# Kernel tuning notes

Measured on AMD Instinct MI355X. Metric: run time of the kernel, lower is better.

The kernel has to match this reference:

```python
import jax, jax.numpy as jnp
import numpy as np

SEQ_LEN = 96      # args.seq_len (in_feats)
H_FEATS = 100
OUT_FEATS = 128
HEADS = 4
K = 64            # args.input_size = nodes per graph
B = 256           # number of graphs (batch_size)
N = K * B
DEG = 8
E = N * DEG
OUT_SIZE = 24     # args.output_size
NEG_SLOPE = 0.2   # PyG GATConv default


def setup_inputs() -> dict:
    key = jax.random.key(0)
    ks = jax.random.split(key, 20)
    s = 0.05
    x = jax.random.normal(ks[0], (N, SEQ_LEN), jnp.float32)
    # intra-graph random edges (dst repeated, src within same graph)
    dst = jnp.repeat(jnp.arange(N, dtype=jnp.int32), DEG)
    src = (dst // K) * K + jax.random.randint(ks[1], (E,), 0, K, dtype=jnp.int32)
    edge_index = jnp.stack([src, dst])
    batch = jnp.repeat(jnp.arange(B, dtype=jnp.int32), K)
    y = jax.random.normal(ks[2], (N, OUT_SIZE), jnp.float32)
    # GATConv 1: in=96 -> heads=4, ch=100
    W1 = jax.random.normal(ks[3], (SEQ_LEN, HEADS * H_FEATS), jnp.float32) * s
    as1 = jax.random.normal(ks[4], (HEADS, H_FEATS), jnp.float32) * s
    ad1 = jax.random.normal(ks[5], (HEADS, H_FEATS), jnp.float32) * s
    b1 = jnp.zeros((H_FEATS,), jnp.float32)
    # GATConv 2: in=100 -> heads=4, ch=128
    W2 = jax.random.normal(ks[6], (H_FEATS, HEADS * OUT_FEATS), jnp.float32) * s
    as2 = jax.random.normal(ks[7], (HEADS, OUT_FEATS), jnp.float32) * s
    ad2 = jax.random.normal(ks[8], (HEADS, OUT_FEATS), jnp.float32) * s
    b2 = jnp.zeros((OUT_FEATS,), jnp.float32)
    # per-node-index MLPs (batched over K)
    fw1 = jax.random.normal(ks[9], (K, OUT_FEATS, 64), jnp.float32) * s
    fb1 = jnp.zeros((K, 64), jnp.float32)
    fw2 = jax.random.normal(ks[10], (K, 64, OUT_SIZE), jnp.float32) * s
    fb2 = jnp.zeros((K, OUT_SIZE), jnp.float32)
    return dict(x=x, edge_index=edge_index, batch=batch, y=y,
                W1=W1, as1=as1, ad1=ad1, b1=b1,
                W2=W2, as2=as2, ad2=ad2, b2=b2,
                fw1=fw1, fb1=fb1, fw2=fw2, fb2=fb2)


def gat_conv(x, src, dst, W, a_src, a_dst, bias):
    # PyG GATConv (concat=False): linear -> per-edge attention -> softmax over
    # incoming edges of each dst -> weighted sum -> mean over heads + bias.
    n = x.shape[0]
    xl = (x @ W).reshape(n, HEADS, -1)                      # [N,H,C]
    al_src = jnp.sum(xl * a_src, axis=-1)                   # [N,H]
    al_dst = jnp.sum(xl * a_dst, axis=-1)                   # [N,H]
    alpha = jax.nn.leaky_relu(al_src[src] + al_dst[dst], NEG_SLOPE)  # [E,H]
    m = jax.ops.segment_max(alpha, dst, num_segments=n)
    ea = jnp.exp(alpha - m[dst])
    denom = jax.ops.segment_sum(ea, dst, num_segments=n)
    w = ea / (denom[dst] + 1e-16)                           # [E,H]
    msg = xl[src] * w[:, :, None]                           # [E,H,C]
    out = jax.ops.segment_sum(msg, dst, num_segments=n)     # [N,H,C]
    return out.mean(axis=1) + bias                          # concat=False


def reference(x, edge_index, batch, y, W1, as1, ad1, b1, W2, as2, ad2, b2, fw1, fb1, fw2, fb2):
    n = x.shape[0]
    src, dst = edge_index[0], edge_index[1]
    loop = jnp.arange(n, dtype=src.dtype)                   # GATConv adds self-loops
    src = jnp.concatenate([src, loop])
    dst = jnp.concatenate([dst, loop])
    h = jax.nn.elu(gat_conv(x, src, dst, W1, as1, ad1, b1))
    h = gat_conv(h, src, dst, W2, as2, ad2, b2)             # [N,128]
    # batch is sorted with K nodes per graph -> stacking == static reshape
    xg = h.reshape(B, K, OUT_FEATS).transpose(1, 0, 2)      # [K,B,128]
    hid = jax.nn.relu(jnp.einsum('kbi,kih->kbh', xg, fw1) + fb1[:, None, :])
    pred = jnp.einsum('kbh,kho->kbo', hid, fw2) + fb2[:, None, :]  # [K,B,out]
    yg = y.reshape(B, K, OUT_SIZE)                          # [B,K,out]
    return pred, yg
```

## Files before the change

kernel.cpp:

```cpp
#include <hip/hip_runtime.h>
#include <hip/hip_bf16.h>
#include <math.h>


#define N_NODES 16384
#define B_GRAPHS 256
#define K_NODES 64
#define DEG 8
#define NHEADS 4
#define C1 100
#define C2 128
#define IN_F 96
#define HID 64
#define OUT_SZ 24
#define PRED_ELEMS (K_NODES * B_GRAPHS * OUT_SZ)

#define W1T_ROWS 448
#define W1T_K    96
#define W2T_ROWS 528
#define W2T_K    128

using bf16 = __hip_bfloat16;
typedef __attribute__((ext_vector_type(8))) short          frag_ab;
typedef __attribute__((ext_vector_type(4))) float          frag_cd;
typedef unsigned short us8 __attribute__((ext_vector_type(8)));
typedef unsigned short us4 __attribute__((ext_vector_type(4)));

__device__ __forceinline__ float us2f(unsigned short u) {
  return __bfloat162float(__ushort_as_bfloat16(u));
}
__device__ __forceinline__ short f2bf_s(float f) {
  return __builtin_bit_cast(short, __float2bfloat16(f));
}

#define P1N  (W1T_ROWS * W1T_K)
#define P2N  (W2T_ROWS * W2T_K)
#define YG4  (PRED_ELEMS / 4)
#define FW1N (K_NODES * HID * C2)
#define FW2N (K_NODES * 32 * HID)
#define PREP_TOT (P1N + P2N + YG4 + FW1N + FW2N)

__global__ __launch_bounds__(256)
void prep(const float* __restrict__ W1, const float* __restrict__ W2,
          const float* __restrict__ y,
          const float* __restrict__ as1, const float* __restrict__ ad1,
          const float* __restrict__ as2, const float* __restrict__ ad2,
          const float* __restrict__ fw1, const float* __restrict__ fw2,
          bf16* __restrict__ W1t, bf16* __restrict__ W2t,
          bf16* __restrict__ fw1t, bf16* __restrict__ fw2t,
          float* __restrict__ yg) {
  int idx = blockIdx.x * 256 + threadIdx.x;
  if (idx < P1N) {
    int c = idx / W1T_K, k = idx - c * W1T_K;
    float v = 0.f;
    if (c < 400) {
      v = W1[(size_t)k * 400 + c];
    } else if (c < 408) {
      int h = (c - 400) & 3;
      const float* av = (c < 404) ? as1 : ad1;
      float s = 0.f;
#pragma unroll 4
      for (int q = 0; q < 100; ++q)
        s += W1[(size_t)k * 400 + h * 100 + q] * av[h * 100 + q];
      v = s;
    }
    W1t[idx] = __float2bfloat16(v);
  } else if (idx < P1N + P2N) {
    int i2 = idx - P1N;
    int c = i2 >> 7, kk = i2 & 127;
    float v = 0.f;
    if (c < 512) {
      if (kk < 100) v = W2[(size_t)kk * 512 + c];
    } else if (c < 520 && kk < 100) {
      int h = (c - 512) & 3;
      const float* av = (c < 516) ? as2 : ad2;
      float s = 0.f;
#pragma unroll 4
      for (int q = 0; q < 128; ++q)
        s += W2[(size_t)kk * 512 + h * 128 + q] * av[h * 128 + q];
      v = s;
    }
    W2t[i2] = __float2bfloat16(v);
  } else if (idx < P1N + P2N + YG4) {
    int j = idx - P1N - P2N;
    int i = j * 4;
    float4 v = *(const float4*)(y + i);
    v.x = __bfloat162float(__float2bfloat16(v.x));
    v.y = __bfloat162float(__float2bfloat16(v.y));
    v.z = __bfloat162float(__float2bfloat16(v.z));
    v.w = __bfloat162float(__float2bfloat16(v.w));
    *(float4*)(yg + i) = v;
  } else if (idx < P1N + P2N + YG4 + FW1N) {
    int i4 = idx - (P1N + P2N + YG4);
    int k = i4 >> 13, r = i4 & 8191, n = r >> 7, kk = r & 127;
    fw1t[i4] = __float2bfloat16(fw1[(size_t)k * (C2 * HID) + kk * HID + n]);
  } else {
    int i5 = idx - (P1N + P2N + YG4 + FW1N);
    if (i5 < FW2N) {
      int k = i5 >> 11, r = i5 & 2047, n = r >> 6, kk = r & 63;
      fw2t[i5] = __float2bfloat16(
          (n < OUT_SZ) ? fw2[(size_t)k * (HID * OUT_SZ) + kk * OUT_SZ + n] : 0.f);
    }
  }
}

__global__ __launch_bounds__(512)
void gat_fused(const float* __restrict__ x,
               const bf16* __restrict__ W1t, const bf16* __restrict__ W2t,
               const int* __restrict__ esrc,
               const float* __restrict__ b1, const float* __restrict__ b2,
               bf16* __restrict__ h2t) {
  constexpr int LDA1 = IN_F + 8;
  constexpr int LDA2 = 136;
  constexpr int LDT  = 72;

  __shared__ __align__(16) short          As[64 * LDA2];
  __shared__ __align__(16) unsigned short xs[W2T_ROWS * LDT];
  __shared__ __align__(16) short          Ps[NHEADS * 64 * LDT];
  __shared__ float bia1[C1], bia2[C2];
  __shared__ int   edg[K_NODES * DEG];

  const int g = blockIdx.x;
  const int t = threadIdx.x;
  const int wv = t >> 6;
  const int l  = t & 63;
  const int lm = l & 15;
  const int lk = (l >> 4) * 8;
  const int rq = (l >> 4) * 4;

  {
    constexpr int QR = IN_F / 4;
    for (int idx = t; idx < 64 * QR; idx += 512) {
      int m = idx / QR, q = idx - m * QR;
      const float4 v = *(const float4*)(x + ((size_t)(g * 64 + m) * IN_F + q * 4));
      short* d = &As[m * LDA1 + q * 4];
      d[0] = f2bf_s(v.x); d[1] = f2bf_s(v.y); d[2] = f2bf_s(v.z); d[3] = f2bf_s(v.w);
    }
  }
  if (t < C1) bia1[t] = b1[t];
  else if (t >= 128 && t < 128 + C2) bia2[t - 128] = b2[t - 128];
  if (t < K_NODES * DEG) edg[t] = esrc[g * K_NODES * DEG + t] & (K_NODES - 1);
  for (int idx = t; idx < NHEADS * 64 * LDT / 8; idx += 512)
    *(us8*)&Ps[idx * 8] = (us8)0;
  __syncthreads();

  if (wv < 7) {
    const int n0 = wv * 64;
    frag_cd acc[4][4] = {};
#pragma unroll
    for (int ks = 0; ks < IN_F; ks += 32) {
      frag_ab b[4];
#pragma unroll
      for (int nt = 0; nt < 4; ++nt)
        b[nt] = *(const frag_ab*)((const short*)W1t +
                                  (size_t)(n0 + nt * 16 + lm) * W1T_K + ks + lk);
#pragma unroll
      for (int mt = 0; mt < 4; ++mt) {
        frag_ab a = *(const frag_ab*)&As[(mt * 16 + lm) * LDA1 + ks + lk];
#pragma unroll
        for (int nt = 0; nt < 4; ++nt)
          acc[mt][nt] = __builtin_amdgcn_mfma_f32_16x16x32_bf16(a, b[nt],
                                                                acc[mt][nt], 0, 0, 0);
      }
    }
#pragma unroll
    for (int mt = 0; mt < 4; ++mt)
#pragma unroll
      for (int nt = 0; nt < 4; ++nt) {
        const int c4 = n0 + nt * 16 + lm;
        us4 o;
#pragma unroll
        for (int r = 0; r < 4; ++r) o[r] = (unsigned short)f2bf_s(acc[mt][nt][r]);
        *(us4*)&xs[c4 * LDT + mt * 16 + rq] = o;
      }
  }
  __syncthreads();

  if (t < 256) {
    const int n = t >> 2, h = t & 3;
    const float ad = us2f(xs[(404 + h) * LDT + n]);
    int   sv[9];
    float a[9];
#pragma unroll
    for (int j = 0; j < 8; ++j) sv[j] = edg[n * DEG + j];
    sv[8] = n;
#pragma unroll
    for (int j = 0; j < 9; ++j) {
      float v = us2f(xs[(400 + h) * LDT + sv[j]]) + ad;
      a[j] = (v >= 0.f) ? v : 0.2f * v;
    }
    float m = -1e30f;
#pragma unroll
    for (int j = 0; j < 9; ++j) m = fmaxf(m, a[j]);
    float s = 0.f;
#pragma unroll
    for (int j = 0; j < 9; ++j) { a[j] = __expf(a[j] - m); s += a[j]; }
    const float inv = 1.f / (s + 1e-16f);
    short* prow = &Ps[(h * 64 + n) * LDT];
#pragma unroll
    for (int j = 0; j < 9; ++j) {
      float tw = a[j];
#pragma unroll
      for (int i = 0; i < 9; ++i)
        if (i != j && sv[i] == sv[j]) tw += a[i];
      prow[sv[j]] = f2bf_s(tw * inv);
    }
  } else {
    for (int i = t - 256; i < 64 * 28; i += 256) {
      int m = i / 28, kk = 100 + (i - m * 28);
      As[m * LDA2 + kk] = 0;
    }
  }
  __syncthreads();

  {
    const int mw = (wv & 3) * 16;
    const int cg = wv >> 2;
    const int ntb = cg * 4;
    const int nte = (cg == 0) ? 4 : 7;
    frag_cd acc[4] = {};
#pragma unroll
    for (int h = 0; h < NHEADS; ++h)
#pragma unroll
      for (int ks = 0; ks < 64; ks += 32) {
        frag_ab a = *(const frag_ab*)&Ps[(h * 64 + mw + lm) * LDT + ks + lk];
        for (int nt = ntb; nt < nte; ++nt) {
          frag_ab b = *(const frag_ab*)&xs[(h * C1 + nt * 16 + lm) * LDT + ks + lk];
          acc[nt - ntb] = __builtin_amdgcn_mfma_f32_16x16x32_bf16(a, b,
                                                                  acc[nt - ntb], 0, 0, 0);
      }
    }
    for (int nt = ntb; nt < nte; ++nt) {
      const int c = nt * 16 + lm;
      if (c < C1) {
        const float bc = bia1[c];
#pragma unroll
        for (int r = 0; r < 4; ++r) {
          float vv = acc[nt - ntb][r] * 0.25f + bc;
          vv = (vv > 0.f) ? vv : (__expf(vv) - 1.f);
          As[(mw + rq + r) * LDA2 + c] = f2bf_s(vv);
        }
      }
    }
  }
  __syncthreads();

  {
    const int n0 = wv * 64;
    frag_cd acc[4][4] = {};
    frag_cd accL[4] = {};
#pragma unroll
    for (int ks = 0; ks < 128; ks += 32) {
      frag_ab b[4];
#pragma unroll
      for (int nt = 0; nt < 4; ++nt)
        b[nt] = *(const frag_ab*)((const short*)W2t +
                                  (size_t)(n0 + nt * 16 + lm) * W2T_K + ks + lk);
      frag_ab bl;
      if (wv == 0)
        bl = *(const frag_ab*)((const short*)W2t +
                               (size_t)(512 + lm) * W2T_K + ks + lk);
#pragma unroll
      for (int mt = 0; mt < 4; ++mt) {
        frag_ab a = *(const frag_ab*)&As[(mt * 16 + lm) * LDA2 + ks + lk];
#pragma unroll
        for (int nt = 0; nt < 4; ++nt)
          acc[mt][nt] = __builtin_amdgcn_mfma_f32_16x16x32_bf16(a, b[nt],
                                                                acc[mt][nt], 0, 0, 0);
        if (wv == 0)
          accL[mt] = __builtin_amdgcn_mfma_f32_16x16x32_bf16(a, bl, accL[mt], 0, 0, 0);
      }
    }
#pragma unroll
    for (int mt = 0; mt < 4; ++mt)
#pragma unroll
      for (int nt = 0; nt < 4; ++nt) {
        const int c4 = n0 + nt * 16 + lm;
        us4 o;
#pragma unroll
        for (int r = 0; r < 4; ++r) o[r] = (unsigned short)f2bf_s(acc[mt][nt][r]);
        *(us4*)&xs[c4 * LDT + mt * 16 + rq] = o;
      }
    if (wv == 0) {
#pragma unroll
      for (int mt = 0; mt < 4; ++mt) {
        us4 o;
#pragma unroll
        for (int r = 0; r < 4; ++r) o[r] = (unsigned short)f2bf_s(accL[mt][r]);
        *(us4*)&xs[(512 + lm) * LDT + mt * 16 + rq] = o;
      }
    }
  }
  __syncthreads();

  if (t < 256) {
    const int n = t >> 2, h = t & 3;
    const float ad = us2f(xs[(516 + h) * LDT + n]);
    int   sv[9];
    float a[9];
#pragma unroll
    for (int j = 0; j < 8; ++j) sv[j] = edg[n * DEG + j];
    sv[8] = n;
#pragma unroll
    for (int j = 0; j < 9; ++j) {
      float v = us2f(xs[(512 + h) * LDT + sv[j]]) + ad;
      a[j] = (v >= 0.f) ? v : 0.2f * v;
    }
    float m = -1e30f;
#pragma unroll
    for (int j = 0; j < 9; ++j) m = fmaxf(m, a[j]);
    float s = 0.f;
#pragma unroll
    for (int j = 0; j < 9; ++j) { a[j] = __expf(a[j] - m); s += a[j]; }
    const float inv = 1.f / (s + 1e-16f);
    short* prow = &Ps[(h * 64 + n) * LDT];
#pragma unroll
    for (int j = 0; j < 9; ++j) {
      float tw = a[j];
#pragma unroll
      for (int i = 0; i < 9; ++i)
        if (i != j && sv[i] == sv[j]) tw += a[i];
      prow[sv[j]] = f2bf_s(tw * inv);
    }
  }
  __syncthreads();

  {
    const int mw = (wv & 3) * 16;
    const int cg = wv >> 2;
    const int ntb = cg * 4;
    frag_cd acc[4] = {};
#pragma unroll
    for (int h = 0; h < NHEADS; ++h)
#pragma unroll
      for (int ks = 0; ks < 64; ks += 32) {
        frag_ab a = *(const frag_ab*)&Ps[(h * 64 + mw + lm) * LDT + ks + lk];
#pragma unroll
        for (int nt = 0; nt < 4; ++nt) {
          frag_ab b = *(const frag_ab*)&xs[(h * C2 + (ntb + nt) * 16 + lm) * LDT + ks + lk];
          acc[nt] = __builtin_amdgcn_mfma_f32_16x16x32_bf16(a, b, acc[nt], 0, 0, 0);
        }
      }
    unsigned short* outp = (unsigned short*)h2t;
#pragma unroll
    for (int nt = 0; nt < 4; ++nt) {
      const int c = (ntb + nt) * 16 + lm;
      const float bc = bia2[c];
#pragma unroll
      for (int r = 0; r < 4; ++r) {
        float vv = acc[nt][r] * 0.25f + bc;
        outp[((size_t)(mw + rq + r) * B_GRAPHS + g) * C2 + c] =
            (unsigned short)f2bf_s(vv);
      }
    }
  }
}

__global__ __launch_bounds__(256)
void mlp_mfma(const bf16* __restrict__ h2t,
              const bf16* __restrict__ fw1t, const float* __restrict__ fb1,
              const bf16* __restrict__ fw2t, const float* __restrict__ fb2,
              float* __restrict__ pred) {
  constexpr int LDH = HID + 8;
  __shared__ __align__(16) short Hs[64 * LDH];

  const int k  = blockIdx.x & 63;
  const int ms = blockIdx.x >> 6;
  const int t  = threadIdx.x;
  const int wv = t >> 6;
  const int l  = t & 63;
  const int lm = l & 15;
  const int lk = (l >> 4) * 8;
  const int rq = (l >> 4) * 4;

  const unsigned short* A  = (const unsigned short*)h2t +
                             ((size_t)k * B_GRAPHS + ms * 64) * C2;
  const unsigned short* B1 = (const unsigned short*)fw1t + (size_t)k * (HID * C2);

  frag_cd acc[4] = {};
#pragma unroll
  for (int ks = 0; ks < C2; ks += 32) {
    frag_ab a = *(const frag_ab*)(A + (size_t)(wv * 16 + lm) * C2 + ks + lk);
#pragma unroll
    for (int nt = 0; nt < 4; ++nt) {
      frag_ab b = *(const frag_ab*)(B1 + (size_t)(nt * 16 + lm) * C2 + ks + lk);
      acc[nt] = __builtin_amdgcn_mfma_f32_16x16x32_bf16(a, b, acc[nt], 0, 0, 0);
    }
  }
#pragma unroll
  for (int nt = 0; nt < 4; ++nt) {
    const int j  = nt * 16 + lm;
    const float bj = fb1[k * HID + j];
#pragma unroll
    for (int r = 0; r < 4; ++r) {
      const int m = wv * 16 + rq + r;
      Hs[m * LDH + j] = f2bf_s(fmaxf(acc[nt][r] + bj, 0.f));
    }
  }
  __syncthreads();

  const unsigned short* B2 = (const unsigned short*)fw2t + (size_t)k * (32 * HID);
  frag_cd acc2[2] = {};
#pragma unroll
  for (int ks = 0; ks < HID; ks += 32) {
    frag_ab a = *(const frag_ab*)&Hs[(wv * 16 + lm) * LDH + ks + lk];
#pragma unroll
    for (int nt = 0; nt < 2; ++nt) {
      frag_ab b = *(const frag_ab*)(B2 + (size_t)(nt * 16 + lm) * HID + ks + lk);
      acc2[nt] = __builtin_amdgcn_mfma_f32_16x16x32_bf16(a, b, acc2[nt], 0, 0, 0);
    }
  }
#pragma unroll
  for (int nt = 0; nt < 2; ++nt) {
    const int q = nt * 16 + lm;
    if (q < OUT_SZ) {
      const float bq = fb2[k * OUT_SZ + q];
#pragma unroll
      for (int r = 0; r < 4; ++r) {
        const int m = wv * 16 + rq + r;
        pred[((size_t)k * B_GRAPHS + ms * 64 + m) * OUT_SZ + q] = acc2[nt][r] + bq;
      }
    }
  }
}

extern "C" void kernel_launch(void* const* d_in, const int* in_sizes, int n_in,
                              void* d_out, int out_size, void* d_ws, size_t ws_size,
                              hipStream_t stream) {
  const float* x   = (const float*)d_in[0];
  const int*   ei  = (const int*)d_in[1];
  const float* y   = (const float*)d_in[3];
  const float* W1  = (const float*)d_in[4];
  const float* as1 = (const float*)d_in[5];
  const float* ad1 = (const float*)d_in[6];
  const float* b1  = (const float*)d_in[7];
  const float* W2  = (const float*)d_in[8];
  const float* as2 = (const float*)d_in[9];
  const float* ad2 = (const float*)d_in[10];
  const float* b2  = (const float*)d_in[11];
  const float* fw1 = (const float*)d_in[12];
  const float* fb1 = (const float*)d_in[13];
  const float* fw2 = (const float*)d_in[14];
  const float* fb2 = (const float*)d_in[15];

  bf16* h2t  = (bf16*)d_ws;
  bf16* W1t  = h2t + (size_t)N_NODES * C2;
  bf16* W2t  = W1t + P1N;
  bf16* fw1t = W2t + P2N;
  bf16* fw2t = fw1t + FW1N;

  float* out = (float*)d_out;

  prep<<<(PREP_TOT + 255) / 256, 256, 0, stream>>>(
      W1, W2, y, as1, ad1, as2, ad2, fw1, fw2, W1t, W2t, fw1t, fw2t,
      out + PRED_ELEMS);

  gat_fused<<<B_GRAPHS, 512, 0, stream>>>(x, W1t, W2t, ei, b1, b2, h2t);

  mlp_mfma<<<K_NODES * 4, 256, 0, stream>>>(h2t, fw1t, fb1, fw2t, fb2, out);
}
```

Baseline: 118.5 us.

## Fuse prep, GAT and MLP kernels into one cooperative kernel with grid syncs

Merges the three launches (weight prep, fused GAT, per-node MLP) into a single cooperative kernel of 256 blocks. Prep work is done in a grid-stride loop while each block stages its graph inputs, and grid-wide syncs replace the kernel boundaries before the GAT GEMMs and before the MLP. The MLP stage is remapped onto 8 waves per block and reuses the As shared buffer. This removes launch overhead and inter-kernel gaps, but adds grid-barrier cost and requires all 256 blocks to be co-resident.

```diff
diff --git a/kernel.cpp b/kernel.cpp
--- a/kernel.cpp
+++ b/kernel.cpp
@@ -1,6 +1,9 @@
 #include <hip/hip_runtime.h>
 #include <hip/hip_bf16.h>
+#include <hip/hip_cooperative_groups.h>
 #include <math.h>
+
+namespace cg = cooperative_groups;
 
 
 #define N_NODES 16384
@@ -40,79 +43,23 @@
 #define FW2N (K_NODES * 32 * HID)
 #define PREP_TOT (P1N + P2N + YG4 + FW1N + FW2N)
 
-__global__ __launch_bounds__(256)
-void prep(const float* __restrict__ W1, const float* __restrict__ W2,
-          const float* __restrict__ y,
-          const float* __restrict__ as1, const float* __restrict__ ad1,
-          const float* __restrict__ as2, const float* __restrict__ ad2,
-          const float* __restrict__ fw1, const float* __restrict__ fw2,
-          bf16* __restrict__ W1t, bf16* __restrict__ W2t,
-          bf16* __restrict__ fw1t, bf16* __restrict__ fw2t,
-          float* __restrict__ yg) {
-  int idx = blockIdx.x * 256 + threadIdx.x;
-  if (idx < P1N) {
-    int c = idx / W1T_K, k = idx - c * W1T_K;
-    float v = 0.f;
-    if (c < 400) {
-      v = W1[(size_t)k * 400 + c];
-    } else if (c < 408) {
-      int h = (c - 400) & 3;
-      const float* av = (c < 404) ? as1 : ad1;
-      float s = 0.f;
-#pragma unroll 4
-      for (int q = 0; q < 100; ++q)
-        s += W1[(size_t)k * 400 + h * 100 + q] * av[h * 100 + q];
-      v = s;
-    }
-    W1t[idx] = __float2bfloat16(v);
-  } else if (idx < P1N + P2N) {
-    int i2 = idx - P1N;
-    int c = i2 >> 7, kk = i2 & 127;
-    float v = 0.f;
-    if (c < 512) {
-      if (kk < 100) v = W2[(size_t)kk * 512 + c];
-    } else if (c < 520 && kk < 100) {
-      int h = (c - 512) & 3;
-      const float* av = (c < 516) ? as2 : ad2;
-      float s = 0.f;
-#pragma unroll 4
-      for (int q = 0; q < 128; ++q)
-        s += W2[(size_t)kk * 512 + h * 128 + q] * av[h * 128 + q];
-      v = s;
-    }
-    W2t[i2] = __float2bfloat16(v);
-  } else if (idx < P1N + P2N + YG4) {
-    int j = idx - P1N - P2N;
-    int i = j * 4;
-    float4 v = *(const float4*)(y + i);
-    v.x = __bfloat162float(__float2bfloat16(v.x));
-    v.y = __bfloat162float(__float2bfloat16(v.y));
-    v.z = __bfloat162float(__float2bfloat16(v.z));
-    v.w = __bfloat162float(__float2bfloat16(v.w));
-    *(float4*)(yg + i) = v;
-  } else if (idx < P1N + P2N + YG4 + FW1N) {
-    int i4 = idx - (P1N + P2N + YG4);
-    int k = i4 >> 13, r = i4 & 8191, n = r >> 7, kk = r & 127;
-    fw1t[i4] = __float2bfloat16(fw1[(size_t)k * (C2 * HID) + kk * HID + n]);
-  } else {
-    int i5 = idx - (P1N + P2N + YG4 + FW1N);
-    if (i5 < FW2N) {
-      int k = i5 >> 11, r = i5 & 2047, n = r >> 6, kk = r & 63;
-      fw2t[i5] = __float2bfloat16(
-          (n < OUT_SZ) ? fw2[(size_t)k * (HID * OUT_SZ) + kk * OUT_SZ + n] : 0.f);
-    }
-  }
-}
-
 __global__ __launch_bounds__(512)
-void gat_fused(const float* __restrict__ x,
-               const bf16* __restrict__ W1t, const bf16* __restrict__ W2t,
-               const int* __restrict__ esrc,
-               const float* __restrict__ b1, const float* __restrict__ b2,
-               bf16* __restrict__ h2t) {
+void fused_all(const float* __restrict__ x, const int* __restrict__ esrc,
+               const float* __restrict__ y,
+               const float* __restrict__ W1, const float* __restrict__ as1,
+               const float* __restrict__ ad1, const float* __restrict__ b1,
+               const float* __restrict__ W2, const float* __restrict__ as2,
+               const float* __restrict__ ad2, const float* __restrict__ b2,
+               const float* __restrict__ fw1, const float* __restrict__ fb1,
+               const float* __restrict__ fw2, const float* __restrict__ fb2,
+               bf16* __restrict__ W1t, bf16* __restrict__ W2t,
+               bf16* __restrict__ fw1t, bf16* __restrict__ fw2t,
+               bf16* __restrict__ h2t,
+               float* __restrict__ yg, float* __restrict__ pred) {
   constexpr int LDA1 = IN_F + 8;
   constexpr int LDA2 = 136;
   constexpr int LDT  = 72;
+  constexpr int LDH  = 72;
 
   __shared__ __align__(16) short          As[64 * LDA2];
   __shared__ __align__(16) unsigned short xs[W2T_ROWS * LDT];
@@ -142,7 +89,61 @@
   if (t < K_NODES * DEG) edg[t] = esrc[g * K_NODES * DEG + t] & (K_NODES - 1);
   for (int idx = t; idx < NHEADS * 64 * LDT / 8; idx += 512)
     *(us8*)&Ps[idx * 8] = (us8)0;
-  __syncthreads();
+
+  for (int idx = g * 512 + t; idx < PREP_TOT; idx += B_GRAPHS * 512) {
+    if (idx < P1N) {
+      int c = idx / W1T_K, k = idx - c * W1T_K;
+      float v = 0.f;
+      if (c < 400) {
+        v = W1[(size_t)k * 400 + c];
+      } else if (c < 408) {
+        int h = (c - 400) & 3;
+        const float* av = (c < 404) ? as1 : ad1;
+        float s = 0.f;
+#pragma unroll 4
+        for (int q = 0; q < 100; ++q)
+          s += W1[(size_t)k * 400 + h * 100 + q] * av[h * 100 + q];
+        v = s;
+      }
+      W1t[idx] = __float2bfloat16(v);
+    } else if (idx < P1N + P2N) {
+      int i2 = idx - P1N;
+      int c = i2 >> 7, kk = i2 & 127;
+      float v = 0.f;
+      if (c < 512) {
+        if (kk < 100) v = W2[(size_t)kk * 512 + c];
+      } else if (c < 520 && kk < 100) {
+        int h = (c - 512) & 3;
+        const float* av = (c < 516) ? as2 : ad2;
+        float s = 0.f;
+#pragma unroll 4
+        for (int q = 0; q < 128; ++q)
+          s += W2[(size_t)kk * 512 + h * 128 + q] * av[h * 128 + q];
+        v = s;
+      }
+      W2t[i2] = __float2bfloat16(v);
+    } else if (idx < P1N + P2N + YG4) {
+      int j = idx - P1N - P2N;
+      int i = j * 4;
+      float4 v = *(const float4*)(y + i);
+      v.x = __bfloat162float(__float2bfloat16(v.x));
+      v.y = __bfloat162float(__float2bfloat16(v.y));
+      v.z = __bfloat162float(__float2bfloat16(v.z));
+      v.w = __bfloat162float(__float2bfloat16(v.w));
+      *(float4*)(yg + i) = v;
+    } else if (idx < P1N + P2N + YG4 + FW1N) {
+      int i4 = idx - (P1N + P2N + YG4);
+      int k = i4 >> 13, r = i4 & 8191, n = r >> 7, kk = r & 127;
+      fw1t[i4] = __float2bfloat16(fw1[(size_t)k * (C2 * HID) + kk * HID + n]);
+    } else {
+      int i5 = idx - (P1N + P2N + YG4 + FW1N);
+      int k = i5 >> 11, r = i5 & 2047, n = r >> 6, kk = r & 63;
+      fw2t[i5] = __float2bfloat16(
+          (n < OUT_SZ) ? fw2[(size_t)k * (HID * OUT_SZ) + kk * OUT_SZ + n] : 0.f);
+    }
+  }
+  __threadfence();
+  cg::this_grid().sync();
 
   if (wv < 7) {
     const int n0 = wv * 64;
@@ -215,9 +216,9 @@
 
   {
     const int mw = (wv & 3) * 16;
-    const int cg = wv >> 2;
-    const int ntb = cg * 4;
-    const int nte = (cg == 0) ? 4 : 7;
+    const int cg2 = wv >> 2;
+    const int ntb = cg2 * 4;
+    const int nte = (cg2 == 0) ? 4 : 7;
     frag_cd acc[4] = {};
 #pragma unroll
     for (int h = 0; h < NHEADS; ++h)
@@ -327,8 +328,8 @@
 
   {
     const int mw = (wv & 3) * 16;
-    const int cg = wv >> 2;
-    const int ntb = cg * 4;
+    const int cg2 = wv >> 2;
+    const int ntb = cg2 * 4;
     frag_cd acc[4] = {};
 #pragma unroll
     for (int h = 0; h < NHEADS; ++h)
@@ -354,71 +355,56 @@
       }
     }
   }
-}
-
-__global__ __launch_bounds__(256)
-void mlp_mfma(const bf16* __restrict__ h2t,
-              const bf16* __restrict__ fw1t, const float* __restrict__ fb1,
-              const bf16* __restrict__ fw2t, const float* __restrict__ fb2,
-              float* __restrict__ pred) {
-  constexpr int LDH = HID + 8;
-  __shared__ __align__(16) short Hs[64 * LDH];
-
-  const int k  = blockIdx.x & 63;
-  const int ms = blockIdx.x >> 6;
-  const int t  = threadIdx.x;
-  const int wv = t >> 6;
-  const int l  = t & 63;
-  const int lm = l & 15;
-  const int lk = (l >> 4) * 8;
-  const int rq = (l >> 4) * 4;
-
-  const unsigned short* A  = (const unsigned short*)h2t +
-                             ((size_t)k * B_GRAPHS + ms * 64) * C2;
-  const unsigned short* B1 = (const unsigned short*)fw1t + (size_t)k * (HID * C2);
-
-  frag_cd acc[4] = {};
-#pragma unroll
-  for (int ks = 0; ks < C2; ks += 32) {
-    frag_ab a = *(const frag_ab*)(A + (size_t)(wv * 16 + lm) * C2 + ks + lk);
-#pragma unroll
-    for (int nt = 0; nt < 4; ++nt) {
-      frag_ab b = *(const frag_ab*)(B1 + (size_t)(nt * 16 + lm) * C2 + ks + lk);
-      acc[nt] = __builtin_amdgcn_mfma_f32_16x16x32_bf16(a, b, acc[nt], 0, 0, 0);
-    }
-  }
-#pragma unroll
-  for (int nt = 0; nt < 4; ++nt) {
-    const int j  = nt * 16 + lm;
-    const float bj = fb1[k * HID + j];
-#pragma unroll
-    for (int r = 0; r < 4; ++r) {
-      const int m = wv * 16 + rq + r;
-      Hs[m * LDH + j] = f2bf_s(fmaxf(acc[nt][r] + bj, 0.f));
-    }
-  }
-  __syncthreads();
-
-  const unsigned short* B2 = (const unsigned short*)fw2t + (size_t)k * (32 * HID);
-  frag_cd acc2[2] = {};
-#pragma unroll
-  for (int ks = 0; ks < HID; ks += 32) {
-    frag_ab a = *(const frag_ab*)&Hs[(wv * 16 + lm) * LDH + ks + lk];
+  __threadfence();
+  cg::this_grid().sync();
+
+  {
+    const int k  = blockIdx.x & 63;
+    const int ms = blockIdx.x >> 6;
+    const int mt = wv >> 1;
+    const int hf = wv & 1;
+
+    const unsigned short* A  = (const unsigned short*)h2t +
+                               ((size_t)k * B_GRAPHS + ms * 64) * C2;
+    const unsigned short* B1 = (const unsigned short*)fw1t + (size_t)k * (HID * C2);
+
+    frag_cd acc[2] = {};
+#pragma unroll
+    for (int ks = 0; ks < C2; ks += 32) {
+      frag_ab a = *(const frag_ab*)(A + (size_t)(mt * 16 + lm) * C2 + ks + lk);
+#pragma unroll
+      for (int nt = 0; nt < 2; ++nt) {
+        frag_ab b = *(const frag_ab*)(B1 + (size_t)((hf * 2 + nt) * 16 + lm) * C2 + ks + lk);
+        acc[nt] = __builtin_amdgcn_mfma_f32_16x16x32_bf16(a, b, acc[nt], 0, 0, 0);
+      }
+    }
 #pragma unroll
     for (int nt = 0; nt < 2; ++nt) {
-      frag_ab b = *(const frag_ab*)(B2 + (size_t)(nt * 16 + lm) * HID + ks + lk);
-      acc2[nt] = __builtin_amdgcn_mfma_f32_16x16x32_bf16(a, b, acc2[nt], 0, 0, 0);
-    }
-  }
-#pragma unroll
-  for (int nt = 0; nt < 2; ++nt) {
-    const int q = nt * 16 + lm;
+      const int j  = (hf * 2 + nt) * 16 + lm;
+      const float bj = fb1[k * HID + j];
+#pragma unroll
+      for (int r = 0; r < 4; ++r) {
+        const int m = mt * 16 + rq + r;
+        As[m * LDH + j] = f2bf_s(fmaxf(acc[nt][r] + bj, 0.f));
+      }
+    }
+    __syncthreads();
+
+    const unsigned short* B2 = (const unsigned short*)fw2t + (size_t)k * (32 * HID);
+    frag_cd acc2 = {};
+#pragma unroll
+    for (int ks = 0; ks < HID; ks += 32) {
+      frag_ab a = *(const frag_ab*)&As[(mt * 16 + lm) * LDH + ks + lk];
+      frag_ab b = *(const frag_ab*)(B2 + (size_t)(hf * 16 + lm) * HID + ks + lk);
+      acc2 = __builtin_amdgcn_mfma_f32_16x16x32_bf16(a, b, acc2, 0, 0, 0);
+    }
+    const int q = hf * 16 + lm;
     if (q < OUT_SZ) {
       const float bq = fb2[k * OUT_SZ + q];
 #pragma unroll
       for (int r = 0; r < 4; ++r) {
-        const int m = wv * 16 + rq + r;
-        pred[((size_t)k * B_GRAPHS + ms * 64 + m) * OUT_SZ + q] = acc2[nt][r] + bq;
+        const int m = mt * 16 + rq + r;
+        pred[((size_t)k * B_GRAPHS + ms * 64 + m) * OUT_SZ + q] = acc2[r] + bq;
       }
     }
   }
@@ -449,13 +435,18 @@
   bf16* fw1t = W2t + P2N;
   bf16* fw2t = fw1t + FW1N;
 
-  float* out = (float*)d_out;
-
-  prep<<<(PREP_TOT + 255) / 256, 256, 0, stream>>>(
-      W1, W2, y, as1, ad1, as2, ad2, fw1, fw2, W1t, W2t, fw1t, fw2t,
-      out + PRED_ELEMS);
-
-  gat_fused<<<B_GRAPHS, 512, 0, stream>>>(x, W1t, W2t, ei, b1, b2, h2t);
-
-  mlp_mfma<<<K_NODES * 4, 256, 0, stream>>>(h2t, fw1t, fb1, fw2t, fb2, out);
+  float* out  = (float*)d_out;
+  float* pred = out;
+  float* yg   = out + PRED_ELEMS;
+
+  void* args[] = {
+    (void*)&x, (void*)&ei, (void*)&y,
+    (void*)&W1, (void*)&as1, (void*)&ad1, (void*)&b1,
+    (void*)&W2, (void*)&as2, (void*)&ad2, (void*)&b2,
+    (void*)&fw1, (void*)&fb1, (void*)&fw2, (void*)&fb2,
+    (void*)&W1t, (void*)&W2t, (void*)&fw1t, (void*)&fw2t, (void*)&h2t,
+    (void*)&yg, (void*)&pred
+  };
+  hipLaunchCooperativeKernel((void*)fused_all, dim3(B_GRAPHS), dim3(512),
+                             args, 0, stream);
 }
```

Result: slower. 286.2 us (+141.5%).

## Remove prep kernel; convert weights inside GAT and MLP kernels

Applied to the files above, without the earlier changes.

Drops the separate weight-preparation kernel. The GAT kernel now reads fp32 W1/W2 directly with strided scalar loads and computes the attention-projection rows into shared memory per block. The MLP kernel stages transposed bf16 copies of fw1/fw2 in shared memory and also handles the y-to-bf16 round trip. This removes one launch and the intermediate round-trip through global memory, but every block redoes the weight conversion, and W1/W2 are now gathered with uncoalesced strided loads inside the MFMA loop.

```diff
diff --git a/kernel.cpp b/kernel.cpp
--- a/kernel.cpp
+++ b/kernel.cpp
@@ -14,11 +14,7 @@
 #define HID 64
 #define OUT_SZ 24
 #define PRED_ELEMS (K_NODES * B_GRAPHS * OUT_SZ)
-
-#define W1T_ROWS 448
-#define W1T_K    96
-#define W2T_ROWS 528
-#define W2T_K    128
+#define YG4 (PRED_ELEMS / 4)
 
 using bf16 = __hip_bfloat16;
 typedef __attribute__((ext_vector_type(8))) short          frag_ab;
@@ -33,90 +29,24 @@
   return __builtin_bit_cast(short, __float2bfloat16(f));
 }
 
-#define P1N  (W1T_ROWS * W1T_K)
-#define P2N  (W2T_ROWS * W2T_K)
-#define YG4  (PRED_ELEMS / 4)
-#define FW1N (K_NODES * HID * C2)
-#define FW2N (K_NODES * 32 * HID)
-#define PREP_TOT (P1N + P2N + YG4 + FW1N + FW2N)
-
-__global__ __launch_bounds__(256)
-void prep(const float* __restrict__ W1, const float* __restrict__ W2,
-          const float* __restrict__ y,
-          const float* __restrict__ as1, const float* __restrict__ ad1,
-          const float* __restrict__ as2, const float* __restrict__ ad2,
-          const float* __restrict__ fw1, const float* __restrict__ fw2,
-          bf16* __restrict__ W1t, bf16* __restrict__ W2t,
-          bf16* __restrict__ fw1t, bf16* __restrict__ fw2t,
-          float* __restrict__ yg) {
-  int idx = blockIdx.x * 256 + threadIdx.x;
-  if (idx < P1N) {
-    int c = idx / W1T_K, k = idx - c * W1T_K;
-    float v = 0.f;
-    if (c < 400) {
-      v = W1[(size_t)k * 400 + c];
-    } else if (c < 408) {
-      int h = (c - 400) & 3;
-      const float* av = (c < 404) ? as1 : ad1;
-      float s = 0.f;
-#pragma unroll 4
-      for (int q = 0; q < 100; ++q)
-        s += W1[(size_t)k * 400 + h * 100 + q] * av[h * 100 + q];
-      v = s;
-    }
-    W1t[idx] = __float2bfloat16(v);
-  } else if (idx < P1N + P2N) {
-    int i2 = idx - P1N;
-    int c = i2 >> 7, kk = i2 & 127;
-    float v = 0.f;
-    if (c < 512) {
-      if (kk < 100) v = W2[(size_t)kk * 512 + c];
-    } else if (c < 520 && kk < 100) {
-      int h = (c - 512) & 3;
-      const float* av = (c < 516) ? as2 : ad2;
-      float s = 0.f;
-#pragma unroll 4
-      for (int q = 0; q < 128; ++q)
-        s += W2[(size_t)kk * 512 + h * 128 + q] * av[h * 128 + q];
-      v = s;
-    }
-    W2t[i2] = __float2bfloat16(v);
-  } else if (idx < P1N + P2N + YG4) {
-    int j = idx - P1N - P2N;
-    int i = j * 4;
-    float4 v = *(const float4*)(y + i);
-    v.x = __bfloat162float(__float2bfloat16(v.x));
-    v.y = __bfloat162float(__float2bfloat16(v.y));
-    v.z = __bfloat162float(__float2bfloat16(v.z));
-    v.w = __bfloat162float(__float2bfloat16(v.w));
-    *(float4*)(yg + i) = v;
-  } else if (idx < P1N + P2N + YG4 + FW1N) {
-    int i4 = idx - (P1N + P2N + YG4);
-    int k = i4 >> 13, r = i4 & 8191, n = r >> 7, kk = r & 127;
-    fw1t[i4] = __float2bfloat16(fw1[(size_t)k * (C2 * HID) + kk * HID + n]);
-  } else {
-    int i5 = idx - (P1N + P2N + YG4 + FW1N);
-    if (i5 < FW2N) {
-      int k = i5 >> 11, r = i5 & 2047, n = r >> 6, kk = r & 63;
-      fw2t[i5] = __float2bfloat16(
-          (n < OUT_SZ) ? fw2[(size_t)k * (HID * OUT_SZ) + kk * OUT_SZ + n] : 0.f);
-    }
-  }
-}
-
 __global__ __launch_bounds__(512)
 void gat_fused(const float* __restrict__ x,
-               const bf16* __restrict__ W1t, const bf16* __restrict__ W2t,
+               const float* __restrict__ W1, const float* __restrict__ W2,
                const int* __restrict__ esrc,
-               const float* __restrict__ b1, const float* __restrict__ b2,
+               const float* __restrict__ as1, const float* __restrict__ ad1,
+               const float* __restrict__ b1,
+               const float* __restrict__ as2, const float* __restrict__ ad2,
+               const float* __restrict__ b2,
                bf16* __restrict__ h2t) {
   constexpr int LDA1 = IN_F + 8;
   constexpr int LDA2 = 136;
   constexpr int LDT  = 72;
 
   __shared__ __align__(16) short          As[64 * LDA2];
-  __shared__ __align__(16) unsigned short xs[W2T_ROWS * LDT];
+  __shared__ __align__(16) unsigned short xs[528 * LDT];
   __shared__ __align__(16) short          Ps[NHEADS * 64 * LDT];
+  __shared__ __align__(16) short          Wsd1[8 * 96];
+  __shared__ __align__(16) short          Wsd2[8 * 128];
   __shared__ float bia1[C1], bia2[C2];
   __shared__ int   edg[K_NODES * DEG];
 
@@ -142,6 +72,28 @@
   if (t < K_NODES * DEG) edg[t] = esrc[g * K_NODES * DEG + t] & (K_NODES - 1);
   for (int idx = t; idx < NHEADS * 64 * LDT / 8; idx += 512)
     *(us8*)&Ps[idx * 8] = (us8)0;
+  for (int e = t; e < 8 * 96; e += 512) {
+    int cc = e / 96, k = e - cc * 96;
+    int h = cc & 3;
+    const float* av = (cc < 4) ? as1 : ad1;
+    float s = 0.f;
+#pragma unroll 4
+    for (int c = 0; c < 100; ++c)
+      s += W1[(size_t)k * 400 + h * 100 + c] * av[h * 100 + c];
+    Wsd1[cc * 96 + k] = f2bf_s(s);
+  }
+  for (int e = t; e < 8 * 128; e += 512) {
+    int cc = e >> 7, kk = e & 127;
+    float s = 0.f;
+    if (kk < 100) {
+      int h = cc & 3;
+      const float* av = (cc < 4) ? as2 : ad2;
+#pragma unroll 4
+      for (int c = 0; c < 128; ++c)
+        s += W2[(size_t)kk * 512 + h * 128 + c] * av[h * 128 + c];
+    }
+    Wsd2[cc * 128 + kk] = f2bf_s(s);
+  }
   __syncthreads();
 
   if (wv < 7) {
@@ -151,9 +103,20 @@
     for (int ks = 0; ks < IN_F; ks += 32) {
       frag_ab b[4];
 #pragma unroll
-      for (int nt = 0; nt < 4; ++nt)
-        b[nt] = *(const frag_ab*)((const short*)W1t +
-                                  (size_t)(n0 + nt * 16 + lm) * W1T_K + ks + lk);
+      for (int nt = 0; nt < 4; ++nt) {
+        const int c = n0 + nt * 16 + lm;
+        frag_ab bb;
+        if (c < 400) {
+#pragma unroll
+          for (int j = 0; j < 8; ++j)
+            bb[j] = f2bf_s(W1[(size_t)(ks + lk + j) * 400 + c]);
+        } else if (c < 408) {
+          bb = *(const frag_ab*)&Wsd1[(c - 400) * 96 + ks + lk];
+        } else {
+          bb = (frag_ab)(short)0;
+        }
+        b[nt] = bb;
+      }
 #pragma unroll
       for (int mt = 0; mt < 4; ++mt) {
         frag_ab a = *(const frag_ab*)&As[(mt * 16 + lm) * LDA1 + ks + lk];
@@ -215,9 +178,9 @@
 
   {
     const int mw = (wv & 3) * 16;
-    const int cg = wv >> 2;
-    const int ntb = cg * 4;
-    const int nte = (cg == 0) ? 4 : 7;
+    const int cg2 = wv >> 2;
+    const int ntb = cg2 * 4;
+    const int nte = (cg2 == 0) ? 4 : 7;
     frag_cd acc[4] = {};
 #pragma unroll
     for (int h = 0; h < NHEADS; ++h)
@@ -253,13 +216,19 @@
     for (int ks = 0; ks < 128; ks += 32) {
       frag_ab b[4];
 #pragma unroll
-      for (int nt = 0; nt < 4; ++nt)
-        b[nt] = *(const frag_ab*)((const short*)W2t +
-                                  (size_t)(n0 + nt * 16 + lm) * W2T_K + ks + lk);
-      frag_ab bl;
-      if (wv == 0)
-        bl = *(const frag_ab*)((const short*)W2t +
-                               (size_t)(512 + lm) * W2T_K + ks + lk);
+      for (int nt = 0; nt < 4; ++nt) {
+        const int c = n0 + nt * 16 + lm;
+        frag_ab bb;
+#pragma unroll
+        for (int j = 0; j < 8; ++j) {
+          const int kk = ks + lk + j;
+          bb[j] = (kk < 100) ? f2bf_s(W2[(size_t)kk * 512 + c]) : (short)0;
+        }
+        b[nt] = bb;
+      }
+      frag_ab bl = (frag_ab)(short)0;
+      if (wv == 0 && lm < 8)
+        bl = *(const frag_ab*)&Wsd2[lm * 128 + ks + lk];
 #pragma unroll
       for (int mt = 0; mt < 4; ++mt) {
         frag_ab a = *(const frag_ab*)&As[(mt * 16 + lm) * LDA2 + ks + lk];
@@ -327,8 +296,8 @@
 
   {
     const int mw = (wv & 3) * 16;
-    const int cg = wv >> 2;
-    const int ntb = cg * 4;
+    const int cg2 = wv >> 2;
+    const int ntb = cg2 * 4;
     frag_cd acc[4] = {};
 #pragma unroll
     for (int h = 0; h < NHEADS; ++h)
@@ -358,10 +327,15 @@
 
 __global__ __launch_bounds__(256)
 void mlp_mfma(const bf16* __restrict__ h2t,
-              const bf16* __restrict__ fw1t, const float* __restrict__ fb1,
-              const bf16* __restrict__ fw2t, const float* __restrict__ fb2,
-              float* __restrict__ pred) {
-  constexpr int LDH = HID + 8;
+              const float* __restrict__ fw1, const float* __restrict__ fb1,
+              const float* __restrict__ fw2, const float* __restrict__ fb2,
+              const float* __restrict__ y,
+              float* __restrict__ yg, float* __restrict__ pred) {
+  constexpr int LDB1 = C2 + 8;
+  constexpr int LDB2 = HID + 8;
+  constexpr int LDH  = HID + 8;
+  __shared__ __align__(16) short B1[HID * LDB1];
+  __shared__ __align__(16) short B2[32 * LDB2];
   __shared__ __align__(16) short Hs[64 * LDH];
 
   const int k  = blockIdx.x & 63;
@@ -373,18 +347,41 @@
   const int lk = (l >> 4) * 8;
   const int rq = (l >> 4) * 4;
 
-  const unsigned short* A  = (const unsigned short*)h2t +
-                             ((size_t)k * B_GRAPHS + ms * 64) * C2;
-  const unsigned short* B1 = (const unsigned short*)fw1t + (size_t)k * (HID * C2);
+  const unsigned short* A = (const unsigned short*)h2t +
+                            ((size_t)k * B_GRAPHS + ms * 64) * C2;
+
+  frag_ab a_pre[4];
+#pragma unroll
+  for (int ksi = 0; ksi < 4; ++ksi)
+    a_pre[ksi] = *(const frag_ab*)(A + (size_t)(wv * 16 + lm) * C2 + ksi * 32 + lk);
+
+  for (int idx = t; idx < C2 * HID; idx += 256) {
+    int kk = idx >> 6, n = idx & 63;
+    B1[n * LDB1 + kk] = f2bf_s(fw1[(size_t)k * (C2 * HID) + idx]);
+  }
+  for (int idx = t; idx < HID * 32; idx += 256) {
+    int kk = idx >> 5, n = idx & 31;
+    B2[n * LDB2 + kk] = f2bf_s(
+        (n < OUT_SZ) ? fw2[(size_t)k * (HID * OUT_SZ) + kk * OUT_SZ + n] : 0.f);
+  }
+  for (int j = blockIdx.x * 256 + t; j < YG4; j += 256 * 256) {
+    int i = j * 4;
+    float4 v = *(const float4*)(y + i);
+    v.x = __bfloat162float(__float2bfloat16(v.x));
+    v.y = __bfloat162float(__float2bfloat16(v.y));
+    v.z = __bfloat162float(__float2bfloat16(v.z));
+    v.w = __bfloat162float(__float2bfloat16(v.w));
+    *(float4*)(yg + i) = v;
+  }
+  __syncthreads();
 
   frag_cd acc[4] = {};
 #pragma unroll
-  for (int ks = 0; ks < C2; ks += 32) {
-    frag_ab a = *(const frag_ab*)(A + (size_t)(wv * 16 + lm) * C2 + ks + lk);
+  for (int ksi = 0; ksi < 4; ++ksi) {
 #pragma unroll
     for (int nt = 0; nt < 4; ++nt) {
-      frag_ab b = *(const frag_ab*)(B1 + (size_t)(nt * 16 + lm) * C2 + ks + lk);
-      acc[nt] = __builtin_amdgcn_mfma_f32_16x16x32_bf16(a, b, acc[nt], 0, 0, 0);
+      frag_ab b = *(const frag_ab*)&B1[(nt * 16 + lm) * LDB1 + ksi * 32 + lk];
+      acc[nt] = __builtin_amdgcn_mfma_f32_16x16x32_bf16(a_pre[ksi], b, acc[nt], 0, 0, 0);
     }
   }
 #pragma unroll
@@ -399,14 +396,13 @@
   }
   __syncthreads();
 
-  const unsigned short* B2 = (const unsigned short*)fw2t + (size_t)k * (32 * HID);
   frag_cd acc2[2] = {};
 #pragma unroll
   for (int ks = 0; ks < HID; ks += 32) {
     frag_ab a = *(const frag_ab*)&Hs[(wv * 16 + lm) * LDH + ks + lk];
 #pragma unroll
     for (int nt = 0; nt < 2; ++nt) {
-      frag_ab b = *(const frag_ab*)(B2 + (size_t)(nt * 16 + lm) * HID + ks + lk);
+      frag_ab b = *(const frag_ab*)&B2[(nt * 16 + lm) * LDB2 + ks + lk];
       acc2[nt] = __builtin_amdgcn_mfma_f32_16x16x32_bf16(a, b, acc2[nt], 0, 0, 0);
     }
   }
@@ -443,19 +439,15 @@
   const float* fw2 = (const float*)d_in[14];
   const float* fb2 = (const float*)d_in[15];
 
-  bf16* h2t  = (bf16*)d_ws;
-  bf16* W1t  = h2t + (size_t)N_NODES * C2;
-  bf16* W2t  = W1t + P1N;
-  bf16* fw1t = W2t + P2N;
-  bf16* fw2t = fw1t + FW1N;
-
-  float* out = (float*)d_out;
-
-  prep<<<(PREP_TOT + 255) / 256, 256, 0, stream>>>(
-      W1, W2, y, as1, ad1, as2, ad2, fw1, fw2, W1t, W2t, fw1t, fw2t,
-      out + PRED_ELEMS);
-
-  gat_fused<<<B_GRAPHS, 512, 0, stream>>>(x, W1t, W2t, ei, b1, b2, h2t);
-
-  mlp_mfma<<<K_NODES * 4, 256, 0, stream>>>(h2t, fw1t, fb1, fw2t, fb2, out);
+  bf16* h2t = (bf16*)d_ws;
+
+  float* out  = (float*)d_out;
+  float* pred = out;
+  float* yg   = out + PRED_ELEMS;
+
+  gat_fused<<<B_GRAPHS, 512, 0, stream>>>(x, W1, W2, ei,
+                                          as1, ad1, b1, as2, ad2, b2, h2t);
+
+  mlp_mfma<<<K_NODES * 4, 256, 0, stream>>>(h2t, fw1, fb1, fw2, fb2, y,
+                                            yg, pred);
 }
```

Result: slower. 151.1 us (+27.5%).
